# Kernel optimization log

Measured on AMD Instinct MI355X. Metric: run time of the kernel, lower is better.

## Reference

```python
import jax, jax.numpy as jnp
import numpy as np

S, N, E = 12, 16384, 262144        # timesteps, nodes, edges per timestep
DIN = DOUT = H = 128               # gcn in/out dim == lstm hidden (required by module)
B = 64                             # batch_size; N % B == 0


def setup_inputs() -> dict:
    key = jax.random.key(0)
    ks = jax.random.split(key, 10)
    return {
        "adj_indices": jax.random.randint(ks[0], (S, 2, E), 0, N, dtype=jnp.int32),
        "adj_values": jax.random.uniform(ks[1], (S, E), dtype=jnp.float32),
        "xs": jax.random.normal(ks[2], (S, N, DIN), dtype=jnp.float32),
        "gcn_weight": jax.random.normal(ks[3], (DIN, DOUT), dtype=jnp.float32) * 0.05,
        "gcn_bias": jnp.zeros((DOUT,), jnp.float32),
        "w_ih": jax.random.normal(ks[4], (4 * H, DOUT), dtype=jnp.float32) * 0.05,
        "w_hh": jax.random.normal(ks[5], (4 * H, H), dtype=jnp.float32) * 0.05,
        "b_ih": jnp.zeros((4 * H,), jnp.float32),
        "b_hh": jnp.zeros((4 * H,), jnp.float32),
        "h0": jax.random.normal(ks[6], (B, H), dtype=jnp.float32),
        "c0": jax.random.normal(ks[7], (B, H), dtype=jnp.float32),
    }


def reference(adj_indices, adj_values, xs, gcn_weight, gcn_bias,
              w_ih, w_hh, b_ih, b_hh, h0, c0):
    # --- GCN per timestep: relu(sparse_A @ (X @ W) + b) ---
    def gcn(idx, vals, x):
        support = x @ gcn_weight                      # [N, DOUT]
        msg = vals[:, None] * support[idx[1]]         # gather cols -> [E, DOUT]
        out = jax.ops.segment_sum(msg, idx[0], num_segments=N)  # scatter rows
        return jax.nn.relu(out + gcn_bias)

    cur = jax.vmap(gcn)(adj_indices, adj_values, xs)  # [S, N, DOUT]
    seq = cur.reshape(-1, B, DOUT)                    # [T=S*N/B, B, H]

    # --- single-layer LSTM (torch gate order: i, f, g, o) ---
    def step(carry, x_t):
        h, c = carry
        gates = x_t @ w_ih.T + b_ih + h @ w_hh.T + b_hh   # [B, 4H]
        i, f, g, o = jnp.split(gates, 4, axis=-1)
        c = jax.nn.sigmoid(f) * c + jax.nn.sigmoid(i) * jnp.tanh(g)
        h = jax.nn.sigmoid(o) * jnp.tanh(c)
        return (h, c), h

    _, hs = jax.lax.scan(step, (h0, c0), seq)         # [T, B, H]
    return hs
```

## Files before the change

kernel.cpp:

```cpp
#include <hip/hip_runtime.h>
#include <cstdint>
#include <cstddef>

#define SS 12
#define NN 16384
#define EE 262144
#define TT 3072

typedef _Float16 h2_t __attribute__((ext_vector_type(2)));
typedef short bf16x8 __attribute__((ext_vector_type(8)));
typedef float floatx4 __attribute__((ext_vector_type(4)));
typedef unsigned short ushortx8 __attribute__((ext_vector_type(8)));

__device__ __forceinline__ float fast_sig(float x) {
    float e = __builtin_amdgcn_exp2f(-1.442695041f * x);
    return __builtin_amdgcn_rcpf(1.f + e);
}
__device__ __forceinline__ float fast_tanh(float x) {
    float e = __builtin_amdgcn_exp2f(2.885390082f * x);
    return 1.f - 2.f * __builtin_amdgcn_rcpf(e + 1.f);
}
__device__ __forceinline__ unsigned short f2bf(float f) {
    unsigned int x = __float_as_uint(f);
    unsigned int r = (x + 0x7FFFu + ((x >> 16) & 1u)) >> 16;
    return (unsigned short)r;
}
__device__ __forceinline__ float bf2f(unsigned short u) {
    return __uint_as_float(((unsigned int)u) << 16);
}
__device__ __forceinline__ h2_t u2h(unsigned int u) {
    union { unsigned int u; h2_t h; } c; c.u = u; return c.h;
}
__device__ __forceinline__ float dpp_xor1(float x) {
    int i = __builtin_amdgcn_mov_dpp(__float_as_int(x), 0xB1, 0xF, 0xF, true);
    return __int_as_float(i);
}

__global__ void k_zero(int* __restrict__ p) {
    p[blockIdx.x * 256 + threadIdx.x] = 0;
}

__global__ void k_count(const int* __restrict__ adj, int* __restrict__ counts) {
    int i = blockIdx.x * 256 + threadIdx.x;
    int t = i / EE, e = i - t * EE;
    int dst = adj[(size_t)t * 2 * EE + e];
    atomicAdd(&counts[t * NN + dst], 1);
}

__global__ void k_scan(const int* __restrict__ counts, int* __restrict__ offs,
                       int* __restrict__ cursor) {
    __shared__ int sums[1024];
    int t = blockIdx.x, tid = threadIdx.x;
    const int per = NN / 1024;
    int base = t * NN + tid * per;
    int local[16];
    int s = 0;
#pragma unroll
    for (int i = 0; i < per; i++) { local[i] = counts[base + i]; s += local[i]; }
    sums[tid] = s;
    __syncthreads();
    for (int off = 1; off < 1024; off <<= 1) {
        int v = (tid >= off) ? sums[tid - off] : 0;
        __syncthreads();
        sums[tid] += v;
        __syncthreads();
    }
    int run = sums[tid] - s;
#pragma unroll
    for (int i = 0; i < per; i++) { offs[base + i] = run; cursor[base + i] = run; run += local[i]; }
}

__global__ void k_scatter(const int* __restrict__ adj, const float* __restrict__ vals,
                          int* __restrict__ cursor, int2* __restrict__ edges) {
    int i = blockIdx.x * 256 + threadIdx.x;
    int t = i / EE, e = i - t * EE;
    int dst = adj[(size_t)t * 2 * EE + e];
    int src = adj[(size_t)t * 2 * EE + EE + e];
    float v = vals[(size_t)t * EE + e];
    int p = atomicAdd(&cursor[t * NN + dst], 1);
    edges[(size_t)t * EE + p] = make_int2(src, __float_as_int(v));
}

__global__ __launch_bounds__(256) void k_support(const float* __restrict__ xs,
                                                 const float* __restrict__ W,
                                                 unsigned short* __restrict__ sup) {
    __shared__ float Ash[64][128];
    __shared__ float Wsh[128][128];
    int tid = threadIdx.x;
    size_t rowbase = (size_t)blockIdx.x * 64;
    const float4* xa = (const float4*)(xs + rowbase * 128);
    float4* As = (float4*)&Ash[0][0];
#pragma unroll
    for (int q = 0; q < 8; q++) As[tid + q * 256] = xa[tid + q * 256];
    const float4* wg = (const float4*)W;
    float4* Ws = (float4*)&Wsh[0][0];
#pragma unroll
    for (int q = 0; q < 16; q++) Ws[tid + q * 256] = wg[tid + q * 256];
    __syncthreads();
    int jg = tid & 31, rg = tid >> 5;
    float acc[8][4];
#pragma unroll
    for (int i = 0; i < 8; i++)
#pragma unroll
        for (int j = 0; j < 4; j++) acc[i][j] = 0.f;
    for (int k4 = 0; k4 < 128; k4 += 4) {
        float4 a[8];
#pragma unroll
        for (int i = 0; i < 8; i++) a[i] = *(const float4*)&Ash[rg * 8 + i][k4];
#pragma unroll
        for (int kk = 0; kk < 4; kk++) {
            float4 wv = *(const float4*)&Wsh[k4 + kk][jg * 4];
#pragma unroll
            for (int i = 0; i < 8; i++) {
                float av = (kk == 0) ? a[i].x : (kk == 1) ? a[i].y : (kk == 2) ? a[i].z : a[i].w;
                acc[i][0] += av * wv.x; acc[i][1] += av * wv.y;
                acc[i][2] += av * wv.z; acc[i][3] += av * wv.w;
            }
        }
    }
#pragma unroll
    for (int i = 0; i < 8; i++) {
        ushort4 o;
        o.x = f2bf(acc[i][0]); o.y = f2bf(acc[i][1]);
        o.z = f2bf(acc[i][2]); o.w = f2bf(acc[i][3]);
        *(ushort4*)&sup[(rowbase + rg * 8 + i) * 128 + jg * 4] = o;
    }
}

__global__ __launch_bounds__(256) void k_gather(const int2* __restrict__ edges,
                         const int* __restrict__ offs,
                         const int* __restrict__ ends,
                         const unsigned short* __restrict__ sup,
                         const float* __restrict__ bias,
                         unsigned short* __restrict__ cur) {
    int bn = blockIdx.x * 4 + (threadIdx.x >> 6);
    bn = __builtin_amdgcn_readfirstlane(bn);
    int t = bn >> 14;
    int l = threadIdx.x & 63;
    int beg = offs[bn];
    int end = ends[bn];
    const unsigned short* supt = sup + (size_t)t * NN * 128;
    const int2* eg = edges + (size_t)t * EE;
    float acc0 = 0.f, acc1 = 0.f;
    int p = beg;
    for (; p + 3 < end; p += 4) {
        int2 e0 = eg[p], e1 = eg[p + 1], e2 = eg[p + 2], e3 = eg[p + 3];
        unsigned int u0 = *(const unsigned int*)&supt[(size_t)e0.x * 128 + 2 * l];
        unsigned int u1 = *(const unsigned int*)&supt[(size_t)e1.x * 128 + 2 * l];
        unsigned int u2 = *(const unsigned int*)&supt[(size_t)e2.x * 128 + 2 * l];
        unsigned int u3 = *(const unsigned int*)&supt[(size_t)e3.x * 128 + 2 * l];
        float w0 = __int_as_float(e0.y), w1 = __int_as_float(e1.y);
        float w2 = __int_as_float(e2.y), w3 = __int_as_float(e3.y);
        acc0 += w0 * bf2f((unsigned short)u0); acc1 += w0 * bf2f((unsigned short)(u0 >> 16));
        acc0 += w1 * bf2f((unsigned short)u1); acc1 += w1 * bf2f((unsigned short)(u1 >> 16));
        acc0 += w2 * bf2f((unsigned short)u2); acc1 += w2 * bf2f((unsigned short)(u2 >> 16));
        acc0 += w3 * bf2f((unsigned short)u3); acc1 += w3 * bf2f((unsigned short)(u3 >> 16));
    }
    for (; p < end; p++) {
        int2 e0 = eg[p];
        unsigned int u0 = *(const unsigned int*)&supt[(size_t)e0.x * 128 + 2 * l];
        float w0 = __int_as_float(e0.y);
        acc0 += w0 * bf2f((unsigned short)u0);
        acc1 += w0 * bf2f((unsigned short)(u0 >> 16));
    }
    float r0 = acc0 + bias[2 * l];
    float r1 = acc1 + bias[2 * l + 1];
    ushort2 o;
    o.x = f2bf(r0 > 0.f ? r0 : 0.f);
    o.y = f2bf(r1 > 0.f ? r1 : 0.f);
    *(ushort2*)&cur[(size_t)bn * 128 + 2 * l] = o;
}

__global__ __launch_bounds__(256) void k_xgates(const unsigned short* __restrict__ cur,
                                                const float* __restrict__ wih,
                                                const float* __restrict__ bih,
                                                const float* __restrict__ bhh,
                                                unsigned short* __restrict__ gx) {
    __shared__ __align__(16) unsigned short At[64][136];
    __shared__ __align__(16) unsigned short Bt[64][136];
    int tid = threadIdx.x;
    size_t rowbase = (size_t)blockIdx.x * 64;
    int gbase = blockIdx.y * 64;
#pragma unroll
    for (int q = 0; q < 4; q++) {
        int idx = tid + q * 256;
        int r = idx >> 4;
        int cc = (idx & 15) * 8;
        *(ushortx8*)&At[r][cc] = *(const ushortx8*)&cur[(rowbase + r) * 128 + cc];
    }
#pragma unroll
    for (int q = 0; q < 8; q++) {
        int idx = tid + q * 256;
        int r = idx >> 5;
        int c4 = (idx & 31) * 4;
        float4 v = *(const float4*)&wih[(size_t)(gbase + r) * 128 + c4];
        ushort4 o;
        o.x = f2bf(v.x); o.y = f2bf(v.y); o.z = f2bf(v.z); o.w = f2bf(v.w);
        *(ushort4*)&Bt[r][c4] = o;
    }
    __syncthreads();
    int wave = tid >> 6, lane = tid & 63;
    int m0 = wave * 16;
    int rin = lane & 15;
    int koff = (lane >> 4) * 8;
    floatx4 acc[4];
#pragma unroll
    for (int n = 0; n < 4; n++) acc[n] = (floatx4){0.f, 0.f, 0.f, 0.f};
#pragma unroll
    for (int kc = 0; kc < 4; kc++) {
        bf16x8 a = *(const bf16x8*)&At[m0 + rin][kc * 32 + koff];
#pragma unroll
        for (int n = 0; n < 4; n++) {
            bf16x8 b = *(const bf16x8*)&Bt[n * 16 + rin][kc * 32 + koff];
            acc[n] = __builtin_amdgcn_mfma_f32_16x16x32_bf16(a, b, acc[n], 0, 0, 0);
        }
    }
    int rq = (lane >> 4) * 4;
#pragma unroll
    for (int n = 0; n < 4; n++) {
        int gcol = gbase + n * 16 + rin;
        float bs = bih[gcol] + bhh[gcol];
        int qg = gcol >> 7, jj = gcol & 127;
        int slot = ((qg >> 1) << 8) | ((jj >> 5) << 6) | ((jj & 31) << 1) | (qg & 1);
#pragma unroll
        for (int i = 0; i < 4; i++) {
            size_t row = rowbase + m0 + rq + i;
            gx[row * 512 + slot] = f2bf(acc[n][i] + bs);
        }
    }
}

__global__ __launch_bounds__(256, 1) void k_lstm(const unsigned short* __restrict__ gx,
                                                 const float* __restrict__ whh,
                                                 const float* __restrict__ h0,
                                                 const float* __restrict__ c0,
                                                 float* __restrict__ out) {
    __shared__ __align__(8) _Float16 hsh[2][128];
    int b = blockIdx.x, tid = threadIdx.x;
    int l = tid & 63, w = tid >> 6;
    int j = w * 32 + (l >> 1);
    bool even = (l & 1) == 0;
    int gate0 = even ? j : 128 + j;
    int gate1 = even ? 256 + j : 384 + j;
    float Ss = even ? 2.f : 1.f;
    float Aa = even ? 2.f : 1.f;
    float Bb = even ? -1.f : 0.f;

    h2_t w0[64], w1[64];
    {
        const float4* r0p = (const float4*)(whh + (size_t)gate0 * 128);
        const float4* r1p = (const float4*)(whh + (size_t)gate1 * 128);
#pragma unroll
        for (int q = 0; q < 32; q++) {
            float4 v = r0p[q];
            h2_t p0; p0.x = (_Float16)v.x; p0.y = (_Float16)v.y;
            h2_t p1; p1.x = (_Float16)v.z; p1.y = (_Float16)v.w;
            w0[2 * q] = p0; w0[2 * q + 1] = p1;
        }
#pragma unroll
        for (int q = 0; q < 32; q++) {
            float4 v = r1p[q];
            h2_t p0; p0.x = (_Float16)v.x; p0.y = (_Float16)v.y;
            h2_t p1; p1.x = (_Float16)v.z; p1.y = (_Float16)v.w;
            w1[2 * q] = p0; w1[2 * q + 1] = p1;
        }
    }
    float c = c0[(size_t)b * 128 + j];
    if (tid < 128) hsh[0][tid] = (_Float16)h0[(size_t)b * 128 + tid];
    __syncthreads();

    unsigned short nA0 = gx[(size_t)b * 512 + tid];
    unsigned short nA1 = gx[(size_t)b * 512 + 256 + tid];
    unsigned short nB0 = gx[((size_t)64 + b) * 512 + tid];
    unsigned short nB1 = gx[((size_t)64 + b) * 512 + 256 + tid];

#define LSTM_STEP(T, RD, WR)                                               \
    {                                                                      \
        unsigned int hv = *(const unsigned int*)&hsh[RD][2 * l];           \
        float px0 = bf2f(nA0), px1 = bf2f(nA1);                            \
        int tp2 = ((T) + 2 < TT) ? (T) + 2 : TT - 1;                       \
        const unsigned short* gp = gx + ((size_t)tp2 * 64 + b) * 512;      \
        unsigned short nC0 = gp[tid];                                      \
        unsigned short nC1 = gp[tid + 256];                                \
        float a00 = 0.f, a01 = 0.f, a10 = 0.f, a11 = 0.f;                  \
        _Pragma("unroll")                                                  \
        for (int mm = 0; mm < 64; mm += 2) {                               \
            unsigned int s0 = __builtin_amdgcn_readlane(hv, mm);           \
            unsigned int s1 = __builtin_amdgcn_readlane(hv, mm + 1);       \
            a00 = __builtin_amdgcn_fdot2(w0[mm], u2h(s0), a00, false);     \
            a10 = __builtin_amdgcn_fdot2(w1[mm], u2h(s0), a10, false);     \
            a01 = __builtin_amdgcn_fdot2(w0[mm + 1], u2h(s1), a01, false); \
            a11 = __builtin_amdgcn_fdot2(w1[mm + 1], u2h(s1), a11, false); \
        }                                                                  \
        float r0 = a00 + a01 + px0;                                        \
        float r1 = a10 + a11 + px1;                                        \
        float act0 = fast_sig(r0);                                         \
        float act1 = Aa * fast_sig(Ss * r1) + Bb;                          \
        float q0 = dpp_xor1(act0);                                         \
        float q1 = dpp_xor1(act1);                                         \
        float gi = even ? act0 : q0;                                       \
        float gf = even ? q0 : act0;                                       \
        float gg = even ? act1 : q1;                                       \
        float go = even ? q1 : act1;                                       \
        c = gf * c + gi * gg;                                              \
        float hn = go * fast_tanh(c);                                      \
        if (even) {                                                        \
            hsh[WR][j] = (_Float16)hn;                                     \
            out[((size_t)(T) * 64 + b) * 128 + j] = hn;                    \
        }                                                                  \
        __syncthreads();                                                   \
        nA0 = nB0; nA1 = nB1; nB0 = nC0; nB1 = nC1;                        \
    }

    for (int t = 0; t < TT; t += 2) {
        LSTM_STEP(t, 0, 1);
        LSTM_STEP(t + 1, 1, 0);
    }
#undef LSTM_STEP
}

extern "C" void kernel_launch(void* const* d_in, const int* in_sizes, int n_in,
                              void* d_out, int out_size, void* d_ws, size_t ws_size,
                              hipStream_t stream) {
    const int* adj    = (const int*)d_in[0];
    const float* vals = (const float*)d_in[1];
    const float* xs   = (const float*)d_in[2];
    const float* gw   = (const float*)d_in[3];
    const float* gb   = (const float*)d_in[4];
    const float* wih  = (const float*)d_in[5];
    const float* whh  = (const float*)d_in[6];
    const float* bih  = (const float*)d_in[7];
    const float* bhh  = (const float*)d_in[8];
    const float* h0   = (const float*)d_in[9];
    const float* c0   = (const float*)d_in[10];
    float* out = (float*)d_out;

    char* ws = (char*)d_ws;
    unsigned short* cur = (unsigned short*)(ws);
    unsigned short* gx  = (unsigned short*)(ws + 50331648);
    unsigned short* sup = (unsigned short*)(ws + 50331648);
    int* counts         = (int*)(ws + 100663296);
    int* offs           = (int*)(ws + 101449728);
    int* cursor         = (int*)(ws + 102236160);
    int2* edges         = (int2*)(ws + 103022592);

    k_zero<<<(SS * NN) / 256, 256, 0, stream>>>(counts);
    k_count<<<(SS * EE) / 256, 256, 0, stream>>>(adj, counts);
    k_scan<<<SS, 1024, 0, stream>>>(counts, offs, cursor);
    k_scatter<<<(SS * EE) / 256, 256, 0, stream>>>(adj, vals, cursor, edges);
    k_support<<<(SS * NN) / 64, 256, 0, stream>>>(xs, gw, sup);
    k_gather<<<(SS * NN) / 4, 256, 0, stream>>>(edges, offs, cursor, sup, gb, cur);
    k_xgates<<<dim3((SS * NN) / 64, 8), 256, 0, stream>>>(cur, wih, bih, bhh, gx);
    k_lstm<<<64, 256, 0, stream>>>(gx, whh, h0, c0, out);
}
```

Before: 2.564 ms.

## Split LSTM recurrent dot products across 4-lane K groups with DPP reduction

Reworks the LSTM recurrence so each quad of threads splits the 128-long hidden dot product into four 32-element slices, reading h from LDS directly instead of 64 readlane broadcasts, then reduces partial sums with DPP xor1/xor2. Each thread now holds all four gate weights for its hidden unit, so every gate activation is computed locally without cross-lane exchange. The gx layout is changed to interleave the four gates per unit so one 8-byte load fetches them, prefetched three steps ahead. Output stores are batched every 8 steps. This trades more LDS reads and duplicated activation math for removing the serial scalar readlane chain on the critical path.

Result: faster. 2.330 ms (-9.1%).

```diff
diff --git a/kernel.cpp b/kernel.cpp
--- a/kernel.cpp
+++ b/kernel.cpp
@@ -28,11 +28,12 @@
 __device__ __forceinline__ float bf2f(unsigned short u) {
     return __uint_as_float(((unsigned int)u) << 16);
 }
-__device__ __forceinline__ h2_t u2h(unsigned int u) {
-    union { unsigned int u; h2_t h; } c; c.u = u; return c.h;
-}
 __device__ __forceinline__ float dpp_xor1(float x) {
     int i = __builtin_amdgcn_mov_dpp(__float_as_int(x), 0xB1, 0xF, 0xF, true);
+    return __int_as_float(i);
+}
+__device__ __forceinline__ float dpp_xor2(float x) {
+    int i = __builtin_amdgcn_mov_dpp(__float_as_int(x), 0x4E, 0xF, 0xF, true);
     return __int_as_float(i);
 }
 
@@ -220,8 +221,7 @@
     for (int n = 0; n < 4; n++) {
         int gcol = gbase + n * 16 + rin;
         float bs = bih[gcol] + bhh[gcol];
-        int qg = gcol >> 7, jj = gcol & 127;
-        int slot = ((qg >> 1) << 8) | ((jj >> 5) << 6) | ((jj & 31) << 1) | (qg & 1);
+        int slot = ((gcol & 127) << 2) | (gcol >> 7);
 #pragma unroll
         for (int i = 0; i < 4; i++) {
             size_t row = rowbase + m0 + rq + i;
@@ -235,86 +235,95 @@
                                                  const float* __restrict__ h0,
                                                  const float* __restrict__ c0,
                                                  float* __restrict__ out) {
-    __shared__ __align__(8) _Float16 hsh[2][128];
+    __shared__ __align__(16) _Float16 hsh[2][128];
     int b = blockIdx.x, tid = threadIdx.x;
-    int l = tid & 63, w = tid >> 6;
-    int j = w * 32 + (l >> 1);
-    bool even = (l & 1) == 0;
-    int gate0 = even ? j : 128 + j;
-    int gate1 = even ? 256 + j : 384 + j;
-    float Ss = even ? 2.f : 1.f;
-    float Aa = even ? 2.f : 1.f;
-    float Bb = even ? -1.f : 0.f;
-
-    h2_t w0[64], w1[64];
-    {
-        const float4* r0p = (const float4*)(whh + (size_t)gate0 * 128);
-        const float4* r1p = (const float4*)(whh + (size_t)gate1 * 128);
-#pragma unroll
-        for (int q = 0; q < 32; q++) {
-            float4 v = r0p[q];
-            h2_t p0; p0.x = (_Float16)v.x; p0.y = (_Float16)v.y;
-            h2_t p1; p1.x = (_Float16)v.z; p1.y = (_Float16)v.w;
-            w0[2 * q] = p0; w0[2 * q + 1] = p1;
-        }
-#pragma unroll
-        for (int q = 0; q < 32; q++) {
-            float4 v = r1p[q];
-            h2_t p0; p0.x = (_Float16)v.x; p0.y = (_Float16)v.y;
-            h2_t p1; p1.x = (_Float16)v.z; p1.y = (_Float16)v.w;
-            w1[2 * q] = p0; w1[2 * q + 1] = p1;
+    int Q = tid >> 2;
+    int ll = tid & 3;
+    int p = (tid >> 1) & 1;
+    int j = 2 * Q + p;
+
+    h2_t wreg[8][16];
+#pragma unroll
+    for (int g8 = 0; g8 < 8; g8++) {
+        int row = (g8 & 3) * 128 + 2 * Q + (g8 >> 2);
+        const float4* rp = (const float4*)(whh + (size_t)row * 128 + ll * 32);
+#pragma unroll
+        for (int q4 = 0; q4 < 8; q4++) {
+            float4 v = rp[q4];
+            h2_t a; a.x = (_Float16)v.x; a.y = (_Float16)v.y;
+            h2_t bq; bq.x = (_Float16)v.z; bq.y = (_Float16)v.w;
+            wreg[g8][2 * q4] = a; wreg[g8][2 * q4 + 1] = bq;
         }
     }
     float c = c0[(size_t)b * 128 + j];
     if (tid < 128) hsh[0][tid] = (_Float16)h0[(size_t)b * 128 + tid];
     __syncthreads();
 
-    unsigned short nA0 = gx[(size_t)b * 512 + tid];
-    unsigned short nA1 = gx[(size_t)b * 512 + 256 + tid];
-    unsigned short nB0 = gx[((size_t)64 + b) * 512 + tid];
-    unsigned short nB1 = gx[((size_t)64 + b) * 512 + 256 + tid];
-
-#define LSTM_STEP(T, RD, WR)                                               \
-    {                                                                      \
-        unsigned int hv = *(const unsigned int*)&hsh[RD][2 * l];           \
-        float px0 = bf2f(nA0), px1 = bf2f(nA1);                            \
-        int tp2 = ((T) + 2 < TT) ? (T) + 2 : TT - 1;                       \
-        const unsigned short* gp = gx + ((size_t)tp2 * 64 + b) * 512;      \
-        unsigned short nC0 = gp[tid];                                      \
-        unsigned short nC1 = gp[tid + 256];                                \
-        float a00 = 0.f, a01 = 0.f, a10 = 0.f, a11 = 0.f;                  \
-        _Pragma("unroll")                                                  \
-        for (int mm = 0; mm < 64; mm += 2) {                               \
-            unsigned int s0 = __builtin_amdgcn_readlane(hv, mm);           \
-            unsigned int s1 = __builtin_amdgcn_readlane(hv, mm + 1);       \
-            a00 = __builtin_amdgcn_fdot2(w0[mm], u2h(s0), a00, false);     \
-            a10 = __builtin_amdgcn_fdot2(w1[mm], u2h(s0), a10, false);     \
-            a01 = __builtin_amdgcn_fdot2(w0[mm + 1], u2h(s1), a01, false); \
-            a11 = __builtin_amdgcn_fdot2(w1[mm + 1], u2h(s1), a11, false); \
-        }                                                                  \
-        float r0 = a00 + a01 + px0;                                        \
-        float r1 = a10 + a11 + px1;                                        \
-        float act0 = fast_sig(r0);                                         \
-        float act1 = Aa * fast_sig(Ss * r1) + Bb;                          \
-        float q0 = dpp_xor1(act0);                                         \
-        float q1 = dpp_xor1(act1);                                         \
-        float gi = even ? act0 : q0;                                       \
-        float gf = even ? q0 : act0;                                       \
-        float gg = even ? act1 : q1;                                       \
-        float go = even ? q1 : act1;                                       \
-        c = gf * c + gi * gg;                                              \
-        float hn = go * fast_tanh(c);                                      \
-        if (even) {                                                        \
-            hsh[WR][j] = (_Float16)hn;                                     \
-            out[((size_t)(T) * 64 + b) * 128 + j] = hn;                    \
-        }                                                                  \
-        __syncthreads();                                                   \
-        nA0 = nB0; nA1 = nB1; nB0 = nC0; nB1 = nC1;                        \
-    }
-
-    for (int t = 0; t < TT; t += 2) {
-        LSTM_STEP(t, 0, 1);
-        LSTM_STEP(t + 1, 1, 0);
+    const unsigned short* gxb = gx + (size_t)b * 512 + 4 * j;
+    uint2 rg0 = *(const uint2*)(gxb);
+    uint2 rg1 = *(const uint2*)(gxb + 32768);
+    uint2 rg2 = *(const uint2*)(gxb + 2 * (size_t)32768);
+
+#define LSTM_STEP(T, RD, WR, QIDX)                                          \
+    {                                                                       \
+        const h2_t* hp_ = (const h2_t*)&hsh[RD][32 * ll];                   \
+        h2_t hs_[16];                                                       \
+        _Pragma("unroll")                                                   \
+        for (int kk = 0; kk < 16; kk++) hs_[kk] = hp_[kk];                  \
+        float part_[8];                                                     \
+        _Pragma("unroll")                                                   \
+        for (int g8 = 0; g8 < 8; g8++) part_[g8] = 0.f;                     \
+        _Pragma("unroll")                                                   \
+        for (int kk = 0; kk < 16; kk++) {                                   \
+            _Pragma("unroll")                                               \
+            for (int g8 = 0; g8 < 8; g8++)                                  \
+                part_[g8] = __builtin_amdgcn_fdot2(wreg[g8][kk], hs_[kk],   \
+                                                   part_[g8], false);       \
+        }                                                                   \
+        _Pragma("unroll")                                                   \
+        for (int g8 = 0; g8 < 8; g8++) part_[g8] += dpp_xor1(part_[g8]);    \
+        _Pragma("unroll")                                                   \
+        for (int g8 = 0; g8 < 8; g8++) part_[g8] += dpp_xor2(part_[g8]);    \
+        float si_ = p ? part_[4] : part_[0];                                \
+        float sf_ = p ? part_[5] : part_[1];                                \
+        float sg_ = p ? part_[6] : part_[2];                                \
+        float so_ = p ? part_[7] : part_[3];                                \
+        uint2 gv_ = rg0;                                                    \
+        float ri_ = si_ + bf2f((unsigned short)(gv_.x & 0xffffu));          \
+        float rf_ = sf_ + bf2f((unsigned short)(gv_.x >> 16));              \
+        float rgg_ = sg_ + bf2f((unsigned short)(gv_.y & 0xffffu));         \
+        float ro_ = so_ + bf2f((unsigned short)(gv_.y >> 16));              \
+        float ai_ = fast_sig(ri_);                                          \
+        float af_ = fast_sig(rf_);                                          \
+        float ag_ = fast_tanh(rgg_);                                        \
+        float ao_ = fast_sig(ro_);                                          \
+        c = af_ * c + ai_ * ag_;                                            \
+        float hn_ = ao_ * fast_tanh(c);                                     \
+        hh8[QIDX] = hn_;                                                    \
+        if ((tid & 1) == 0) hsh[WR][j] = (_Float16)hn_;                     \
+        rg0 = rg1; rg1 = rg2;                                               \
+        {                                                                   \
+            int tp_ = ((T) + 3 < TT) ? (T) + 3 : TT - 1;                    \
+            rg2 = *(const uint2*)(gxb + (size_t)tp_ * 32768);               \
+        }                                                                   \
+        __syncthreads();                                                    \
+    }
+
+    for (int t8 = 0; t8 < TT; t8 += 8) {
+        float hh8[8];
+        LSTM_STEP(t8 + 0, 0, 1, 0);
+        LSTM_STEP(t8 + 1, 1, 0, 1);
+        LSTM_STEP(t8 + 2, 0, 1, 2);
+        LSTM_STEP(t8 + 3, 1, 0, 3);
+        LSTM_STEP(t8 + 4, 0, 1, 4);
+        LSTM_STEP(t8 + 5, 1, 0, 5);
+        LSTM_STEP(t8 + 6, 0, 1, 6);
+        LSTM_STEP(t8 + 7, 1, 0, 7);
+        if ((tid & 1) == 0) {
+#pragma unroll
+            for (int q = 0; q < 8; q++)
+                out[((size_t)(t8 + q) * 64 + b) * 128 + j] = hh8[q];
+        }
     }
 #undef LSTM_STEP
 }
```
